# Kernel tuning notes

Measured on AMD Instinct MI355X. Metric: run time of the kernel, lower is better.

The kernel has to match this reference:

```python
import jax, jax.numpy as jnp
import numpy as np

B, C, H, W = 4, 128, 64, 64


def setup_inputs() -> dict:
    key = jax.random.key(0)
    k1, k2 = jax.random.split(key)
    x = jax.random.normal(k1, (B, C, H, W), dtype=jnp.float32)
    # 1x1 conv kv_mapper: weight [C_out, C_in], bias [C_out]; C_out == C_in == C
    W_kv = jax.random.normal(k2, (C, C), dtype=jnp.float32) * (1.0 / np.sqrt(C))
    b_kv = jnp.zeros((C,), dtype=jnp.float32)
    return {"x": x, "W_kv": W_kv, "b_kv": b_kv}


def reference(x, W_kv, b_kv):
    b, c, h, w = x.shape
    # kv_mapper: 1x1 conv  -> v: [b, c, h, w]
    v = jnp.einsum('bchw,oc->bohw', x, W_kv) + b_kv[None, :, None, None]
    # rearrange 'b c h w -> b (h w) c'
    L = h * w
    values = v.reshape(b, c, L).transpose(0, 2, 1)    # keys == values
    queries = x.reshape(b, c, L).transpose(0, 2, 1)
    # scaled dot-product attention, full [b, L, L] scores
    scores = jnp.einsum('blc,btc->blt', queries, values) / jnp.sqrt(jnp.asarray(c, x.dtype))
    attn = jax.nn.softmax(scores, axis=-1)
    out = jnp.einsum('blt,btv->blv', attn, values)    # [b, L, c]
    # rearrange 'b (h w) c -> b c h w'
    return out.transpose(0, 2, 1).reshape(b, c, h, w)
```

## Files before the change

### kernel.cpp

```cpp
#include <hip/hip_runtime.h>

#define LQ 4096
#define CH 128
#define NB 4
#define QSCALE 0.12753139626233174f
#define PSTR 72
#define ASTR 136
#define BSTR 72
#define MAXCH 8

typedef __attribute__((ext_vector_type(8))) unsigned short ushort8;
typedef __attribute__((ext_vector_type(8))) __bf16 bf16x8;
typedef __attribute__((ext_vector_type(4))) float f32x4;

__device__ inline unsigned short f2bf(float f) {
    unsigned int u = __builtin_bit_cast(unsigned int, f);
    u += 0x7fffu + ((u >> 16) & 1u);
    return (unsigned short)(u >> 16);
}
__device__ inline float bf2f(unsigned short h) {
    unsigned int u = (unsigned int)h << 16;
    return __builtin_bit_cast(float, u);
}

__global__ __launch_bounds__(256) void prep_kernel(
    const float* __restrict__ x, const float* __restrict__ Wkv,
    const float* __restrict__ bkv,
    unsigned short* __restrict__ Vt, unsigned short* __restrict__ Vc)
{
    __shared__ unsigned short vs[64 * 64];
    const int tid = threadIdx.x;
    const int lane = tid & 63;
    const int b = blockIdx.x & 3;
    const int l0 = ((blockIdx.x >> 2) & 63) << 6;
    const int ohalf = blockIdx.x >> 8;
    const int o0l = __builtin_amdgcn_readfirstlane((tid >> 6) << 4);

    float xr[CH];
    #pragma unroll
    for (int c = 0; c < CH; ++c)
        xr[c] = x[((size_t)b * CH + c) * LQ + l0 + lane];

    for (int oo = 0; oo < 16; oo += 2) {
        const int ol = o0l + oo;
        const int o = ohalf * 64 + ol;
        const float* wr0 = Wkv + (size_t)o * CH;
        const float* wr1 = wr0 + CH;
        float p0[4] = {bkv[o], 0.f, 0.f, 0.f};
        float p1[4] = {bkv[o + 1], 0.f, 0.f, 0.f};
        #pragma unroll
        for (int c = 0; c < CH; c += 4) {
            #pragma unroll
            for (int k = 0; k < 4; ++k) {
                p0[k] += wr0[c + k] * xr[c + k];
                p1[k] += wr1[c + k] * xr[c + k];
            }
        }
        const float a0 = (p0[0] + p0[1]) + (p0[2] + p0[3]);
        const float a1 = (p1[0] + p1[1]) + (p1[2] + p1[3]);
        const unsigned short h0 = f2bf(a0), h1 = f2bf(a1);
        Vc[((size_t)b * CH + o) * LQ + l0 + lane] = h0;
        Vc[((size_t)b * CH + o + 1) * LQ + l0 + lane] = h1;
        vs[ol * 64 + lane] = h0;
        vs[(ol + 1) * 64 + lane] = h1;
    }
    __syncthreads();
    #pragma unroll
    for (int i = 0; i < 2; ++i) {
        const int idx = i * 256 + tid;
        const int l = idx >> 3, og = idx & 7;
        ushort8 v;
        #pragma unroll
        for (int k = 0; k < 8; ++k) v[k] = vs[(og * 8 + k) * 64 + l];
        *(ushort8*)(Vt + ((size_t)b * LQ + l0 + l) * CH + ohalf * 64 + og * 8) = v;
    }
}

__global__ __launch_bounds__(256, 2) void attn_kernel(
    const float* __restrict__ x, const unsigned short* __restrict__ Vt,
    const unsigned short* __restrict__ Vc,
    unsigned short* __restrict__ Opart, float* __restrict__ Lsum, int titers)
{
    __shared__ __align__(16) unsigned short tileA[64 * ASTR];
    __shared__ __align__(16) unsigned short tileB[128 * BSTR];
    __shared__ __align__(16) unsigned short Plds_all[4][32 * PSTR];
    const int tid = threadIdx.x;
    const int wave = tid >> 6, lane = tid & 63;
    const int quad = lane >> 4, l16 = lane & 15;
    const int b = blockIdx.x & 3;
    const int rest = blockIdx.x >> 2;
    const int qtile = rest & 31;
    const int chunk = rest >> 5;
    const int q0w = (qtile << 7) + (wave << 5);
    const int tbase = chunk * titers * 64;

    const unsigned short* vtb = Vt + (size_t)b * LQ * CH;
    const unsigned short* vcb = Vc + (size_t)b * CH * LQ;

    bf16x8 qf[2][4];
    #pragma unroll
    for (int mt = 0; mt < 2; ++mt)
        #pragma unroll
        for (int kc = 0; kc < 4; ++kc) {
            ushort8 v;
            #pragma unroll
            for (int j = 0; j < 8; ++j) {
                int c = kc * 32 + quad * 8 + j;
                v[j] = f2bf(x[((size_t)b * CH + c) * LQ + q0w + mt * 16 + l16] * QSCALE);
            }
            qf[mt][kc] = __builtin_bit_cast(bf16x8, v);
        }

    f32x4 oacc[2][8];
    #pragma unroll
    for (int mt = 0; mt < 2; ++mt)
        #pragma unroll
        for (int i = 0; i < 8; ++i) oacc[mt][i] = f32x4{0.f, 0.f, 0.f, 0.f};
    float lsum[2][4] = {{0.f, 0.f, 0.f, 0.f}, {0.f, 0.f, 0.f, 0.f}};

    unsigned short* Plds = Plds_all[wave];

    ushort8 RA[4], RB[4];
    {
        const int t0 = tbase;
        #pragma unroll
        for (int i = 0; i < 4; ++i) {
            const int ci = i * 256 + tid;
            RA[i] = *(const ushort8*)(vtb + (size_t)(t0 + (ci >> 4)) * CH + (ci & 15) * 8);
        }
        #pragma unroll
        for (int i = 0; i < 4; ++i) {
            const int ci = i * 256 + tid;
            RB[i] = *(const ushort8*)(vcb + (size_t)(ci >> 3) * LQ + t0 + (ci & 7) * 8);
        }
    }

    for (int it = 0; it < titers; ++it) {
        __syncthreads();
        #pragma unroll
        for (int i = 0; i < 4; ++i) {
            const int ci = i * 256 + tid;
            *(ushort8*)(tileA + (ci >> 4) * ASTR + (ci & 15) * 8) = RA[i];
        }
        #pragma unroll
        for (int i = 0; i < 4; ++i) {
            const int ci = i * 256 + tid;
            *(ushort8*)(tileB + (ci >> 3) * BSTR + (ci & 7) * 8) = RB[i];
        }
        __syncthreads();
        {
            const int t0n = (it + 1 < titers) ? tbase + (it + 1) * 64 : tbase;
            #pragma unroll
            for (int i = 0; i < 4; ++i) {
                const int ci = i * 256 + tid;
                RA[i] = *(const ushort8*)(vtb + (size_t)(t0n + (ci >> 4)) * CH + (ci & 15) * 8);
            }
            #pragma unroll
            for (int i = 0; i < 4; ++i) {
                const int ci = i * 256 + tid;
                RB[i] = *(const ushort8*)(vcb + (size_t)(ci >> 3) * LQ + t0n + (ci & 7) * 8);
            }
        }
        f32x4 s[2][4];
        #pragma unroll
        for (int mt = 0; mt < 2; ++mt)
            #pragma unroll
            for (int nt = 0; nt < 4; ++nt) s[mt][nt] = f32x4{0.f, 0.f, 0.f, 0.f};
        #pragma unroll
        for (int nt = 0; nt < 4; ++nt) {
            bf16x8 vB[4];
            #pragma unroll
            for (int kc = 0; kc < 4; ++kc)
                vB[kc] = __builtin_bit_cast(bf16x8,
                    *(const ushort8*)(tileA + (nt * 16 + l16) * ASTR + kc * 32 + quad * 8));
            #pragma unroll
            for (int mt = 0; mt < 2; ++mt)
                #pragma unroll
                for (int kc = 0; kc < 4; ++kc)
                    s[mt][nt] = __builtin_amdgcn_mfma_f32_16x16x32_bf16(qf[mt][kc], vB[kc], s[mt][nt], 0, 0, 0);
        }
        #pragma unroll
        for (int mt = 0; mt < 2; ++mt)
            #pragma unroll
            for (int nt = 0; nt < 4; ++nt)
                #pragma unroll
                for (int r = 0; r < 4; ++r) {
                    float p = exp2f(s[mt][nt][r]);
                    lsum[mt][r] += p;
                    Plds[(mt * 16 + quad * 4 + r) * PSTR + nt * 16 + l16] = f2bf(p);
                }
        bf16x8 pf[2][2];
        #pragma unroll
        for (int mt = 0; mt < 2; ++mt)
            #pragma unroll
            for (int kt = 0; kt < 2; ++kt)
                pf[mt][kt] = __builtin_bit_cast(bf16x8,
                    *(const ushort8*)(Plds + (mt * 16 + l16) * PSTR + kt * 32 + quad * 8));
        #pragma unroll
        for (int nc = 0; nc < 8; ++nc) {
            #pragma unroll
            for (int kt = 0; kt < 2; ++kt) {
                bf16x8 vC = __builtin_bit_cast(bf16x8,
                    *(const ushort8*)(tileB + (nc * 16 + l16) * BSTR + kt * 32 + quad * 8));
                #pragma unroll
                for (int mt = 0; mt < 2; ++mt)
                    oacc[mt][nc] = __builtin_amdgcn_mfma_f32_16x16x32_bf16(pf[mt][kt], vC, oacc[mt][nc], 0, 0, 0);
            }
        }
    }
    const size_t pbase = ((size_t)(chunk * NB + b) * LQ);
    #pragma unroll
    for (int mt = 0; mt < 2; ++mt)
        #pragma unroll
        for (int r = 0; r < 4; ++r) {
            const int q = q0w + mt * 16 + quad * 4 + r;
            unsigned short* orow = Opart + (pbase + q) * CH + l16;
            #pragma unroll
            for (int nc = 0; nc < 8; ++nc) orow[nc * 16] = f2bf(oacc[mt][nc][r]);
            float v = lsum[mt][r];
            v += __shfl_xor(v, 1);
            v += __shfl_xor(v, 2);
            v += __shfl_xor(v, 4);
            v += __shfl_xor(v, 8);
            if (l16 == 0) Lsum[pbase + q] = v;
        }
}

__global__ __launch_bounds__(256) void combine_kernel(
    const unsigned short* __restrict__ Opart, const float* __restrict__ Lsum,
    float* __restrict__ out, int nchunk)
{
    __shared__ __align__(16) float ls[32 * 132];
    __shared__ float linv[32];
    const int tid = threadIdx.x;
    const int b = blockIdx.x & 3;
    const int q0 = (blockIdx.x >> 2) << 5;

    if (tid < 32) {
        float s = 0.f;
        for (int ch = 0; ch < nchunk; ++ch) s += Lsum[(size_t)(ch * NB + b) * LQ + q0 + tid];
        linv[tid] = 1.0f / s;
    }
    __syncthreads();
    {
        const int c8 = (tid & 15) * 8, qg = tid >> 4;
        #pragma unroll
        for (int i = 0; i < 2; ++i) {
            const int q = qg * 2 + i;
            float s[8];
            #pragma unroll
            for (int k = 0; k < 8; ++k) s[k] = 0.f;
            for (int ch = 0; ch < nchunk; ++ch) {
                ushort8 p = *(const ushort8*)(Opart +
                    ((size_t)(ch * NB + b) * LQ + q0 + q) * CH + c8);
                #pragma unroll
                for (int k = 0; k < 8; ++k) s[k] += bf2f(p[k]);
            }
            const float li = linv[q];
            f32x4 o0, o1;
            #pragma unroll
            for (int k = 0; k < 4; ++k) { o0[k] = s[k] * li; o1[k] = s[k + 4] * li; }
            *(f32x4*)(ls + q * 132 + c8) = o0;
            *(f32x4*)(ls + q * 132 + c8 + 4) = o1;
        }
    }
    __syncthreads();
    {
        const int c = tid & 127, qh = tid >> 7;
        float* dst = out + ((size_t)b * CH + c) * LQ + q0 + qh * 16;
        #pragma unroll
        for (int i = 0; i < 4; ++i) {
            f32x4 o;
            #pragma unroll
            for (int r = 0; r < 4; ++r) o[r] = ls[(qh * 16 + i * 4 + r) * 132 + c];
            ((f32x4*)dst)[i] = o;
        }
    }
}

extern "C" void kernel_launch(void* const* d_in, const int* in_sizes, int n_in,
                              void* d_out, int out_size, void* d_ws, size_t ws_size,
                              hipStream_t stream) {
    const float* x   = (const float*)d_in[0];
    const float* Wkv = (const float*)d_in[1];
    const float* bkv = (const float*)d_in[2];
    float* out = (float*)d_out;

    const size_t vElems = (size_t)NB * LQ * CH;
    unsigned short* Vt = (unsigned short*)d_ws;
    unsigned short* Vc = Vt + vElems;
    float* Lsum = (float*)(Vc + vElems);
    unsigned short* Opart = (unsigned short*)(Lsum + (size_t)MAXCH * NB * LQ);

    int nchunk = 4;
    const size_t fixed = 2 * vElems * 2 + (size_t)MAXCH * NB * LQ * 4;
    while (nchunk > 1 && fixed + (size_t)nchunk * NB * LQ * CH * 2 > ws_size) nchunk >>= 1;
    const int titers = (LQ / 64) / nchunk;

    prep_kernel<<<dim3(512), dim3(256), 0, stream>>>(x, Wkv, bkv, Vt, Vc);
    attn_kernel<<<dim3(128 * nchunk), dim3(256), 0, stream>>>(x, Vt, Vc, Opart, Lsum, titers);
    combine_kernel<<<dim3(512), dim3(256), 0, stream>>>(Opart, Lsum, out, nchunk);
}
```

Baseline: 143.8 us.

## Keep softmax probabilities in registers by computing transposed scores, drop P LDS round-trip

The QK^T product is now computed as K·Q^T, so each lane's accumulator outputs already sit in the layout the PV MFMA needs as its A operand. The probabilities are packed straight into bf16 registers, which removes the per-wave P shared-memory staging and its extra LDS traffic. The PV MFMA is fed only half its K depth, with zero-padded operands, so MFMA issue count doubles. Removing the P buffer frees LDS, so occupancy is raised to 3 blocks per CU and the split count goes up to 8 chunks, adding more partial outputs for the combine step. Rounding uses a cheaper round-half-up bf16 pack and the raw hardware exp2.

```diff
diff --git a/kernel.cpp b/kernel.cpp
--- a/kernel.cpp
+++ b/kernel.cpp
@@ -4,12 +4,12 @@
 #define CH 128
 #define NB 4
 #define QSCALE 0.12753139626233174f
-#define PSTR 72
 #define ASTR 136
 #define BSTR 72
 #define MAXCH 8
 
 typedef __attribute__((ext_vector_type(8))) unsigned short ushort8;
+typedef __attribute__((ext_vector_type(4))) unsigned short ushort4v;
 typedef __attribute__((ext_vector_type(8))) __bf16 bf16x8;
 typedef __attribute__((ext_vector_type(4))) float f32x4;
 
@@ -21,6 +21,11 @@
 __device__ inline float bf2f(unsigned short h) {
     unsigned int u = (unsigned int)h << 16;
     return __builtin_bit_cast(float, u);
+}
+__device__ inline unsigned int bfpack2(float a, float b) {
+    unsigned int ua = __builtin_bit_cast(unsigned int, a) + 0x8000u;
+    unsigned int ub = __builtin_bit_cast(unsigned int, b) + 0x8000u;
+    return (ua >> 16) | (ub & 0xffff0000u);
 }
 
 __global__ __launch_bounds__(256) void prep_kernel(
@@ -76,14 +81,13 @@
     }
 }
 
-__global__ __launch_bounds__(256, 2) void attn_kernel(
+__global__ __launch_bounds__(256, 3) void attn_kernel(
     const float* __restrict__ x, const unsigned short* __restrict__ Vt,
     const unsigned short* __restrict__ Vc,
     unsigned short* __restrict__ Opart, float* __restrict__ Lsum, int titers)
 {
     __shared__ __align__(16) unsigned short tileA[64 * ASTR];
     __shared__ __align__(16) unsigned short tileB[128 * BSTR];
-    __shared__ __align__(16) unsigned short Plds_all[4][32 * PSTR];
     const int tid = threadIdx.x;
     const int wave = tid >> 6, lane = tid & 63;
     const int quad = lane >> 4, l16 = lane & 15;
@@ -116,9 +120,7 @@
     for (int mt = 0; mt < 2; ++mt)
         #pragma unroll
         for (int i = 0; i < 8; ++i) oacc[mt][i] = f32x4{0.f, 0.f, 0.f, 0.f};
-    float lsum[2][4] = {{0.f, 0.f, 0.f, 0.f}, {0.f, 0.f, 0.f, 0.f}};
-
-    unsigned short* Plds = Plds_all[wave];
+    float lsum[2] = {0.f, 0.f};
 
     ushort8 RA[4], RB[4];
     {
@@ -161,54 +163,59 @@
                 RB[i] = *(const ushort8*)(vcb + (size_t)(ci >> 3) * LQ + t0n + (ci & 7) * 8);
             }
         }
-        f32x4 s[2][4];
-        #pragma unroll
-        for (int mt = 0; mt < 2; ++mt)
-            #pragma unroll
-            for (int nt = 0; nt < 4; ++nt) s[mt][nt] = f32x4{0.f, 0.f, 0.f, 0.f};
         #pragma unroll
         for (int nt = 0; nt < 4; ++nt) {
-            bf16x8 vB[4];
+            bf16x8 vA[4];
             #pragma unroll
             for (int kc = 0; kc < 4; ++kc)
-                vB[kc] = __builtin_bit_cast(bf16x8,
+                vA[kc] = __builtin_bit_cast(bf16x8,
                     *(const ushort8*)(tileA + (nt * 16 + l16) * ASTR + kc * 32 + quad * 8));
-            #pragma unroll
-            for (int mt = 0; mt < 2; ++mt)
+            f32x4 s[2];
+            #pragma unroll
+            for (int mt = 0; mt < 2; ++mt) {
+                s[mt] = f32x4{0.f, 0.f, 0.f, 0.f};
                 #pragma unroll
                 for (int kc = 0; kc < 4; ++kc)
-                    s[mt][nt] = __builtin_amdgcn_mfma_f32_16x16x32_bf16(qf[mt][kc], vB[kc], s[mt][nt], 0, 0, 0);
-        }
-        #pragma unroll
-        for (int mt = 0; mt < 2; ++mt)
-            #pragma unroll
-            for (int nt = 0; nt < 4; ++nt)
-                #pragma unroll
-                for (int r = 0; r < 4; ++r) {
-                    float p = exp2f(s[mt][nt][r]);
-                    lsum[mt][r] += p;
-                    Plds[(mt * 16 + quad * 4 + r) * PSTR + nt * 16 + l16] = f2bf(p);
-                }
-        bf16x8 pf[2][2];
-        #pragma unroll
-        for (int mt = 0; mt < 2; ++mt)
-            #pragma unroll
-            for (int kt = 0; kt < 2; ++kt)
-                pf[mt][kt] = __builtin_bit_cast(bf16x8,
-                    *(const ushort8*)(Plds + (mt * 16 + l16) * PSTR + kt * 32 + quad * 8));
-        #pragma unroll
-        for (int nc = 0; nc < 8; ++nc) {
-            #pragma unroll
-            for (int kt = 0; kt < 2; ++kt) {
-                bf16x8 vC = __builtin_bit_cast(bf16x8,
-                    *(const ushort8*)(tileB + (nc * 16 + l16) * BSTR + kt * 32 + quad * 8));
+                    s[mt] = __builtin_amdgcn_mfma_f32_16x16x32_bf16(vA[kc], qf[mt][kc], s[mt], 0, 0, 0);
+            }
+            bf16x8 pf[2];
+            #pragma unroll
+            for (int mt = 0; mt < 2; ++mt) {
+                float p0 = __builtin_amdgcn_exp2f(s[mt][0]);
+                float p1 = __builtin_amdgcn_exp2f(s[mt][1]);
+                float p2 = __builtin_amdgcn_exp2f(s[mt][2]);
+                float p3 = __builtin_amdgcn_exp2f(s[mt][3]);
+                lsum[mt] += (p0 + p1) + (p2 + p3);
+                unsigned int lo = bfpack2(p0, p1);
+                unsigned int hi = bfpack2(p2, p3);
+                ushort8 pk;
+                pk[0] = (unsigned short)lo; pk[1] = (unsigned short)(lo >> 16);
+                pk[2] = (unsigned short)hi; pk[3] = (unsigned short)(hi >> 16);
+                pk[4] = 0; pk[5] = 0; pk[6] = 0; pk[7] = 0;
+                pf[mt] = __builtin_bit_cast(bf16x8, pk);
+            }
+            #pragma unroll
+            for (int nc = 0; nc < 8; ++nc) {
+                ushort4v d = *(const ushort4v*)(tileB +
+                    (nc * 16 + l16) * BSTR + nt * 16 + quad * 4);
+                ushort8 vb;
+                vb[0] = d[0]; vb[1] = d[1]; vb[2] = d[2]; vb[3] = d[3];
+                vb[4] = 0; vb[5] = 0; vb[6] = 0; vb[7] = 0;
+                bf16x8 vB = __builtin_bit_cast(bf16x8, vb);
                 #pragma unroll
                 for (int mt = 0; mt < 2; ++mt)
-                    oacc[mt][nc] = __builtin_amdgcn_mfma_f32_16x16x32_bf16(pf[mt][kt], vC, oacc[mt][nc], 0, 0, 0);
+                    oacc[mt][nc] = __builtin_amdgcn_mfma_f32_16x16x32_bf16(pf[mt], vB, oacc[mt][nc], 0, 0, 0);
             }
         }
     }
     const size_t pbase = ((size_t)(chunk * NB + b) * LQ);
+    #pragma unroll
+    for (int mt = 0; mt < 2; ++mt) {
+        float v = lsum[mt];
+        v += __shfl_xor(v, 16);
+        v += __shfl_xor(v, 32);
+        if (lane < 16) Lsum[pbase + q0w + mt * 16 + lane] = v;
+    }
     #pragma unroll
     for (int mt = 0; mt < 2; ++mt)
         #pragma unroll
@@ -217,12 +224,6 @@
             unsigned short* orow = Opart + (pbase + q) * CH + l16;
             #pragma unroll
             for (int nc = 0; nc < 8; ++nc) orow[nc * 16] = f2bf(oacc[mt][nc][r]);
-            float v = lsum[mt][r];
-            v += __shfl_xor(v, 1);
-            v += __shfl_xor(v, 2);
-            v += __shfl_xor(v, 4);
-            v += __shfl_xor(v, 8);
-            if (l16 == 0) Lsum[pbase + q] = v;
         }
 }
 
@@ -292,7 +293,7 @@
     float* Lsum = (float*)(Vc + vElems);
     unsigned short* Opart = (unsigned short*)(Lsum + (size_t)MAXCH * NB * LQ);
 
-    int nchunk = 4;
+    int nchunk = MAXCH;
     const size_t fixed = 2 * vElems * 2 + (size_t)MAXCH * NB * LQ * 4;
     while (nchunk > 1 && fixed + (size_t)nchunk * NB * LQ * CH * 2 > ws_size) nchunk >>= 1;
     const int titers = (LQ / 64) / nchunk;
```

Measured after the change: 255.6 us. +77.7%, slower.
